# Performance work log

Measured on AMD Instinct MI355X. Metric: run time of the kernel, lower is better.

## Reference

```python
import jax, jax.numpy as jnp
import numpy as np

D_MODEL = 1024
NUM_HEADS = 16
D_K = D_MODEL // NUM_HEADS


def setup_inputs() -> dict:
    key = jax.random.key(0)
    k1, k2, k3, k4 = jax.random.split(key, 4)
    x = jax.random.normal(k1, (2, 2048, D_MODEL), dtype=jnp.float32)
    # qkv_proj: Linear(d_model, 3*d_model, bias=False); stored as [in, out] for x @ W
    W_qkv = jax.random.normal(k2, (D_MODEL, 3 * D_MODEL), dtype=jnp.float32) * (1.0 / np.sqrt(D_MODEL))
    W_out = jax.random.normal(k3, (D_MODEL, D_MODEL), dtype=jnp.float32) * (1.0 / np.sqrt(D_MODEL))
    b_out = jax.random.normal(k4, (D_MODEL,), dtype=jnp.float32) * 0.01
    return {"x": x, "W_qkv": W_qkv, "W_out": W_out, "b_out": b_out}


def reference(x, W_qkv, W_out, b_out):
    B, N, C = x.shape
    scale = 1.0 / np.sqrt(D_K)
    qkv = (x @ W_qkv).reshape(B, N, 3, NUM_HEADS, D_K)
    qkv = jnp.transpose(qkv, (2, 0, 3, 1, 4))  # [3, B, H, N, d_k]
    q, k, v = qkv[0], qkv[1], qkv[2]
    scores = jnp.einsum("bhqd,bhkd->bhqk", q, k) * scale  # [B,H,N,N]
    attn = jax.nn.softmax(scores, axis=-1)
    out = jnp.einsum("bhqk,bhkd->bhqd", attn, v)  # [B,H,N,d_k]
    out = jnp.transpose(out, (0, 2, 1, 3)).reshape(B, N, C)
    return out @ W_out + b_out
```

## Files before the change

kernel.cpp:

```cpp
#include <hip/hip_runtime.h>
#include <cstdint>

typedef __bf16 bf16_t;
typedef __bf16 bf16x4 __attribute__((ext_vector_type(4)));
typedef __bf16 bf16x8 __attribute__((ext_vector_type(8)));
typedef float  f32x4  __attribute__((ext_vector_type(4)));
typedef uint32_t u32x4 __attribute__((ext_vector_type(4)));

#define MFMA16(a,b,c) __builtin_amdgcn_mfma_f32_16x16x32_bf16((a),(b),(c),0,0,0)
#define BAR()    __builtin_amdgcn_s_barrier()
#define VMW(n)   asm volatile("s_waitcnt vmcnt(" #n ")" ::: "memory")

__device__ __forceinline__ void gload_lds16(const bf16_t* g, bf16_t* l) {
  __builtin_amdgcn_global_load_lds(
      (const __attribute__((address_space(1))) unsigned int*)g,
      (__attribute__((address_space(3))) unsigned int*)l,
      16, 0, 0);
}

__device__ __forceinline__ uint32_t cvt_pk_bf16(float lo, float hi) {
  uint32_t r;
  asm("v_cvt_pk_bf16_f32 %0, %1, %2" : "=v"(r) : "v"(lo), "v"(hi));
  return r;
}

__global__ void k_prep(const float* __restrict__ x, bf16_t* __restrict__ xb,
                       const float* __restrict__ Wq, bf16_t* __restrict__ WqT,
                       const float* __restrict__ Wo, bf16_t* __restrict__ WoT) {
  __shared__ float tile[32][33];
  int bid = blockIdx.x;
  if (bid < 2048) {
    int i = bid * blockDim.x + threadIdx.x;
    const float4* p = reinterpret_cast<const float4*>(x) + (size_t)i * 2;
    float4 a = p[0], b = p[1];
    bf16x8 v;
    v[0]=(bf16_t)a.x; v[1]=(bf16_t)a.y; v[2]=(bf16_t)a.z; v[3]=(bf16_t)a.w;
    v[4]=(bf16_t)b.x; v[5]=(bf16_t)b.y; v[6]=(bf16_t)b.z; v[7]=(bf16_t)b.w;
    *reinterpret_cast<bf16x8*>(xb + (size_t)i * 8) = v;
    return;
  }
  int t = bid - 2048;
  int bx = t & 127, k0 = (t >> 7) * 32;
  const float* W; bf16_t* WT; int N, n0;
  if (bx < 96) { W = Wq; WT = WqT; N = 3072; n0 = bx * 32; }
  else         { W = Wo; WT = WoT; N = 1024; n0 = (bx - 96) * 32; }
  int c = threadIdx.x & 31, r8 = threadIdx.x >> 5;
#pragma unroll
  for (int rr = 0; rr < 4; rr++) {
    int r = r8 + rr * 8;
    tile[r][c] = W[(size_t)(k0 + r) * N + n0 + c];
  }
  __syncthreads();
#pragma unroll
  for (int rr = 0; rr < 4; rr++) {
    int r = r8 + rr * 8;
    WT[(size_t)(n0 + r) * 1024 + k0 + c] = (bf16_t)tile[c][r];
  }
}

template<int EPI, int MT, int NT>
__global__ __launch_bounds__(256, 2) void k_gemm(
    const bf16_t* __restrict__ A, const bf16_t* __restrict__ BT, int Klen,
    bf16_t* __restrict__ Qo, bf16_t* __restrict__ Ko, bf16_t* __restrict__ Vt,
    const float* __restrict__ bias, float* __restrict__ Out, int Nout) {
  constexpr int WM = MT / 2;
  constexpr int MF = WM / 16;
  constexpr int WN = NT / 2;
  constexpr int NF = WN / 16;
  __shared__ bf16_t As[2][MT * 32];
  __shared__ bf16_t Bs[2][NT * 32];
  int tid = threadIdx.x, lane = tid & 63, wid = tid >> 6;
  int row0 = blockIdx.x * MT, col0 = blockIdx.y * NT;
  int wr = wid >> 1, wc = wid & 1;
  int g = lane >> 4, li = lane & 15;

  f32x4 acc[MF][NF] = {};

  auto stage = [&](int buf, int kt) {
    int k0 = kt * 32;
#pragma unroll
    for (int j = 0; j < MT / 64; j++) {
      int q = tid + 256 * j;
      int r = q >> 2, part = q & 3;
      gload_lds16(A + (size_t)(row0 + r) * Klen + k0 + part * 8,
                  &As[buf][q * 8]);
    }
#pragma unroll
    for (int j = 0; j < NT / 64; j++) {
      int q = tid + 256 * j;
      int r = q >> 2, part = q & 3;
      gload_lds16(BT + (size_t)(col0 + r) * Klen + k0 + part * 8,
                  &Bs[buf][q * 8]);
    }
  };

  int nk = Klen >> 5;
  stage(0, 0);
  for (int kt = 0; kt < nk; kt++) {
    __syncthreads();
    if (kt + 1 < nk) stage((kt + 1) & 1, kt + 1);
    int buf = kt & 1;
    int kl = g * 8;
    bf16x8 a[MF], b[NF];
#pragma unroll
    for (int m = 0; m < MF; m++)
      a[m] = *reinterpret_cast<const bf16x8*>(&As[buf][(wr * WM + m * 16 + li) * 32 + kl]);
#pragma unroll
    for (int n = 0; n < NF; n++)
      b[n] = *reinterpret_cast<const bf16x8*>(&Bs[buf][(wc * WN + n * 16 + li) * 32 + kl]);
#pragma unroll
    for (int m = 0; m < MF; m++)
#pragma unroll
      for (int n = 0; n < NF; n++)
        acc[m][n] = MFMA16(a[m], b[n], acc[m][n]);
  }

#pragma unroll
  for (int m = 0; m < MF; m++) {
    int rg = row0 + wr * WM + m * 16 + g * 4;
    int b2 = rg >> 11, nn0 = rg & 2047;
#pragma unroll
    for (int n = 0; n < NF; n++) {
      int cg = col0 + wc * WN + n * 16 + li;
      if constexpr (EPI == 0) {
        int t = cg >> 10, h = (cg >> 6) & 15, dk = cg & 63;
        int head = (b2 << 4) + h;
        if (t == 2) {
          bf16x4 pv;
#pragma unroll
          for (int ii = 0; ii < 4; ii++) pv[ii] = (bf16_t)acc[m][n][ii];
          *reinterpret_cast<bf16x4*>(
              &Vt[(size_t)head * 131072 + (size_t)dk * 2048 + nn0]) = pv;
        } else {
#pragma unroll
          for (int ii = 0; ii < 4; ii++) {
            float v = acc[m][n][ii];
            size_t idx = ((size_t)head * 2048 + nn0 + ii) * 64 + dk;
            if (t == 0) Qo[idx] = (bf16_t)(v * 0.18033688011112042f);
            else        Ko[idx] = (bf16_t)v;
          }
        }
      } else {
#pragma unroll
        for (int ii = 0; ii < 4; ii++)
          Out[(size_t)(rg + ii) * Nout + cg] = acc[m][n][ii] + bias[cg];
      }
    }
  }
}

__global__ __launch_bounds__(256, 2) void k_flash(
    const bf16_t* __restrict__ Q, const bf16_t* __restrict__ K,
    const bf16_t* __restrict__ VT, bf16_t* __restrict__ O) {
  __shared__ bf16_t Ks[3][64 * 64];
  __shared__ bf16_t Vs[3][64 * 64];

  int bi = (blockIdx.x & 7) * 64 + (blockIdx.x >> 3);
  int head = bi >> 4, qt = bi & 15;
  int tid = threadIdx.x, lane = tid & 63, wid = tid >> 6;
  int qg = wid >> 1, kg = wid & 1;
  int g = lane >> 4, li = lane & 15;

  const bf16_t* Qh = Q + (size_t)head * 131072 + (size_t)qt * 128 * 64;
  const bf16_t* Kh = K + (size_t)head * 131072;
  const bf16_t* Vh = VT + (size_t)head * 131072;

  bf16x8 qf[4][2];
#pragma unroll
  for (int nq = 0; nq < 4; nq++) {
    const bf16_t* qrow = Qh + (size_t)(qg * 64 + nq * 16 + li) * 64;
    qf[nq][0] = *reinterpret_cast<const bf16x8*>(qrow + g * 8);
    qf[nq][1] = *reinterpret_cast<const bf16x8*>(qrow + 32 + g * 8);
  }

  u32x4 onesw;
  onesw[0] = 0x3F803F80u; onesw[1] = 0x3F803F80u;
  onesw[2] = 0x3F803F80u; onesw[3] = 0x3F803F80u;
  bf16x8 ones = __builtin_bit_cast(bf16x8, onesw);

  f32x4 zero4 = {};
  f32x4 o[4][4] = {};
  f32x4 osum[4] = {};

  auto stage = [&](int buf, int t) {
    int kv0 = t * 64;
#pragma unroll
    for (int j = 0; j < 2; j++) {
      int q = tid + 256 * j;
      int key = q >> 3, part = q & 7;
      int sw = (key & 7) ^ (((key >> 3) & 3) << 1);
      gload_lds16(Kh + (size_t)(kv0 + key) * 64 + ((part ^ sw) * 8),
                  &Ks[buf][(tid + j * 256) * 8]);
    }
#pragma unroll
    for (int j = 0; j < 2; j++) {
      int q = tid + 256 * j;
      int dv = q >> 3, part = q & 7;
      gload_lds16(Vh + (size_t)dv * 2048 + kv0 + ((part ^ (dv & 7)) * 8),
                  &Vs[buf][(tid + j * 256) * 8]);
    }
  };

  stage(0, 0);
  stage(1, 1);
  for (int t = 0; t < 32; t++) {
    if (t < 31) { VMW(4); } else { VMW(0); }
    BAR();
    __builtin_amdgcn_sched_barrier(0);
    if (t + 2 < 32) stage((t + 2) % 3, t + 2);
    int buf = t % 3;
    char* KsB = (char*)&Ks[buf][0];
    char* VsB = (char*)&Vs[buf][0];

    bf16x8 ka[2][2];
#pragma unroll
    for (int kd = 0; kd < 2; kd++)
#pragma unroll
      for (int c = 0; c < 2; c++) {
        int key = kg * 32 + ((li >> 2) << 3) + c * 4 + (li & 3);
        int sw = (key & 7) ^ (((key >> 3) & 3) << 1);
        ka[kd][c] = *reinterpret_cast<const bf16x8*>(
            KsB + key * 128 + (((kd * 4 + g) ^ sw) << 4));
      }

    f32x4 s[2][4];
    __builtin_amdgcn_s_setprio(1);
#pragma unroll
    for (int c = 0; c < 2; c++)
#pragma unroll
      for (int nq = 0; nq < 4; nq++)
        s[c][nq] = MFMA16(ka[0][c], qf[nq][0], zero4);
#pragma unroll
    for (int c = 0; c < 2; c++)
#pragma unroll
      for (int nq = 0; nq < 4; nq++)
        s[c][nq] = MFMA16(ka[1][c], qf[nq][1], s[c][nq]);
    __builtin_amdgcn_s_setprio(0);

    bf16x8 pa[4];
#pragma unroll
    for (int c = 0; c < 2; c++)
#pragma unroll
      for (int nq = 0; nq < 4; nq++)
#pragma unroll
        for (int i = 0; i < 4; i++)
          s[c][nq][i] = __builtin_amdgcn_exp2f(s[c][nq][i]);
#pragma unroll
    for (int nq = 0; nq < 4; nq++) {
      u32x4 w;
      w[0] = cvt_pk_bf16(s[0][nq][0], s[0][nq][1]);
      w[1] = cvt_pk_bf16(s[0][nq][2], s[0][nq][3]);
      w[2] = cvt_pk_bf16(s[1][nq][0], s[1][nq][1]);
      w[3] = cvt_pk_bf16(s[1][nq][2], s[1][nq][3]);
      pa[nq] = __builtin_bit_cast(bf16x8, w);
    }

    __builtin_amdgcn_s_setprio(1);
#pragma unroll
    for (int nq = 0; nq < 4; nq++)
      osum[nq] = MFMA16(pa[nq], ones, osum[nq]);
#pragma unroll
    for (int ndv = 0; ndv < 4; ndv++) {
      int dv = ndv * 16 + li;
      bf16x8 b = *reinterpret_cast<const bf16x8*>(
          VsB + dv * 128 + ((kg * 64 + g * 16) ^ ((dv & 7) << 4)));
#pragma unroll
      for (int nq = 0; nq < 4; nq++)
        o[nq][ndv] = MFMA16(pa[nq], b, o[nq][ndv]);
    }
    __builtin_amdgcn_s_setprio(0);
  }

  __syncthreads();
  float* dump = (float*)&Ks[0][0] + qg * 5120;
  if (kg == 1) {
#pragma unroll
    for (int nq = 0; nq < 4; nq++)
#pragma unroll
      for (int ndv = 0; ndv < 4; ndv++)
#pragma unroll
        for (int i = 0; i < 4; i++)
          dump[(((nq * 4 + ndv) * 4) + i) * 64 + lane] = o[nq][ndv][i];
#pragma unroll
    for (int nq = 0; nq < 4; nq++)
#pragma unroll
      for (int i = 0; i < 4; i++)
        dump[4096 + (nq * 4 + i) * 64 + lane] = osum[nq][i];
  }
  __syncthreads();
  if (kg == 0) {
    int b2 = head >> 4, h = head & 15;
#pragma unroll
    for (int nq = 0; nq < 4; nq++) {
#pragma unroll
      for (int i = 0; i < 4; i++) {
        float ltot = osum[nq][i] + dump[4096 + (nq * 4 + i) * 64 + lane];
        float inv = 1.f / ltot;
        int n = qt * 128 + qg * 64 + nq * 16 + g * 4 + i;
        size_t base = ((size_t)b2 * 2048 + n) * 1024 + h * 64;
#pragma unroll
        for (int ndv = 0; ndv < 4; ndv++) {
          float tot = o[nq][ndv][i] + dump[(((nq * 4 + ndv) * 4) + i) * 64 + lane];
          O[base + ndv * 16 + li] = (bf16_t)(tot * inv);
        }
      }
    }
  }
}

extern "C" void kernel_launch(void* const* d_in, const int* in_sizes, int n_in,
                              void* d_out, int out_size, void* d_ws, size_t ws_size,
                              hipStream_t stream) {
  const float* x    = (const float*)d_in[0];
  const float* Wqkv = (const float*)d_in[1];
  const float* Wout = (const float*)d_in[2];
  const float* bout = (const float*)d_in[3];
  float* out = (float*)d_out;

  char* ws = (char*)d_ws;
  bf16_t* xb    = (bf16_t*)(ws);
  bf16_t* wqkvT = (bf16_t*)(ws + ((size_t)8  << 20));
  bf16_t* woutT = (bf16_t*)(ws + ((size_t)14 << 20));
  bf16_t* qw    = (bf16_t*)(ws + ((size_t)16 << 20));
  bf16_t* kw    = (bf16_t*)(ws + ((size_t)24 << 20));
  bf16_t* vtw   = (bf16_t*)(ws + ((size_t)40 << 20));
  bf16_t* ow    = (bf16_t*)(ws + ((size_t)48 << 20));

  k_prep<<<2048 + 4096, 256, 0, stream>>>(x, xb, Wqkv, wqkvT, Wout, woutT);
  k_gemm<0, 128, 192><<<dim3(32, 16), 256, 0, stream>>>(
      xb, wqkvT, 1024, qw, kw, vtw, nullptr, nullptr, 0);
  k_flash<<<512, 256, 0, stream>>>(qw, kw, vtw, ow);
  k_gemm<1, 64, 128><<<dim3(64, 8), 256, 0, stream>>>(
      ow, woutT, 1024, nullptr, nullptr, nullptr, bout, out, 1024);
}
```

Baseline: 105.6 us.

## Software-pipeline QK of next tile with PV of current tile in flash kernel

Restructures the flash attention loop so the QK^T MFMAs for tile t+1 are issued together with the PV MFMAs for tile t, and the exp/pack of the next tile follows. This is meant to hide exp latency behind matrix work. The LDS ring grows from 3 to 4 buffers and the prefetch distance from 2 to 3, with a prologue and epilogue added. The cost is more LDS per block, which may limit occupancy at 2 blocks per CU, and more live registers.

```diff
diff --git a/kernel.cpp b/kernel.cpp
--- a/kernel.cpp
+++ b/kernel.cpp
@@ -152,8 +152,8 @@
 __global__ __launch_bounds__(256, 2) void k_flash(
     const bf16_t* __restrict__ Q, const bf16_t* __restrict__ K,
     const bf16_t* __restrict__ VT, bf16_t* __restrict__ O) {
-  __shared__ bf16_t Ks[3][64 * 64];
-  __shared__ bf16_t Vs[3][64 * 64];
+  __shared__ bf16_t Ks[4][64 * 64];
+  __shared__ bf16_t Vs[4][64 * 64];
 
   int bi = (blockIdx.x & 7) * 64 + (blockIdx.x >> 3);
   int head = bi >> 4, qt = bi & 15;
@@ -181,6 +181,7 @@
   f32x4 zero4 = {};
   f32x4 o[4][4] = {};
   f32x4 osum[4] = {};
+  bf16x8 pa[4];
 
   auto stage = [&](int buf, int t) {
     int kv0 = t * 64;
@@ -201,18 +202,7 @@
     }
   };
 
-  stage(0, 0);
-  stage(1, 1);
-  for (int t = 0; t < 32; t++) {
-    if (t < 31) { VMW(4); } else { VMW(0); }
-    BAR();
-    __builtin_amdgcn_sched_barrier(0);
-    if (t + 2 < 32) stage((t + 2) % 3, t + 2);
-    int buf = t % 3;
-    char* KsB = (char*)&Ks[buf][0];
-    char* VsB = (char*)&Vs[buf][0];
-
-    bf16x8 ka[2][2];
+  auto read_ka = [&](char* KsB, bf16x8 ka[2][2]) {
 #pragma unroll
     for (int kd = 0; kd < 2; kd++)
 #pragma unroll
@@ -222,9 +212,8 @@
         ka[kd][c] = *reinterpret_cast<const bf16x8*>(
             KsB + key * 128 + (((kd * 4 + g) ^ sw) << 4));
       }
-
-    f32x4 s[2][4];
-    __builtin_amdgcn_s_setprio(1);
+  };
+  auto qk = [&](bf16x8 ka[2][2], f32x4 s[2][4]) {
 #pragma unroll
     for (int c = 0; c < 2; c++)
 #pragma unroll
@@ -235,9 +224,8 @@
 #pragma unroll
       for (int nq = 0; nq < 4; nq++)
         s[c][nq] = MFMA16(ka[1][c], qf[nq][1], s[c][nq]);
-    __builtin_amdgcn_s_setprio(0);
-
-    bf16x8 pa[4];
+  };
+  auto exp_pack = [&](f32x4 s[2][4]) {
 #pragma unroll
     for (int c = 0; c < 2; c++)
 #pragma unroll
@@ -254,22 +242,58 @@
       w[3] = cvt_pk_bf16(s[1][nq][2], s[1][nq][3]);
       pa[nq] = __builtin_bit_cast(bf16x8, w);
     }
-
-    __builtin_amdgcn_s_setprio(1);
+  };
+  auto pv = [&](char* VsB) {
+    bf16x8 vb[4];
+#pragma unroll
+    for (int ndv = 0; ndv < 4; ndv++) {
+      int dv = ndv * 16 + li;
+      vb[ndv] = *reinterpret_cast<const bf16x8*>(
+          VsB + dv * 128 + ((kg * 64 + g * 16) ^ ((dv & 7) << 4)));
+    }
 #pragma unroll
     for (int nq = 0; nq < 4; nq++)
       osum[nq] = MFMA16(pa[nq], ones, osum[nq]);
 #pragma unroll
-    for (int ndv = 0; ndv < 4; ndv++) {
-      int dv = ndv * 16 + li;
-      bf16x8 b = *reinterpret_cast<const bf16x8*>(
-          VsB + dv * 128 + ((kg * 64 + g * 16) ^ ((dv & 7) << 4)));
+    for (int ndv = 0; ndv < 4; ndv++)
 #pragma unroll
       for (int nq = 0; nq < 4; nq++)
-        o[nq][ndv] = MFMA16(pa[nq], b, o[nq][ndv]);
-    }
+        o[nq][ndv] = MFMA16(pa[nq], vb[ndv], o[nq][ndv]);
+  };
+
+  stage(0, 0); stage(1, 1); stage(2, 2);
+  VMW(8); BAR();
+  __builtin_amdgcn_sched_barrier(0);
+  {
+    bf16x8 ka[2][2];
+    f32x4 s[2][4];
+    read_ka((char*)&Ks[0][0], ka);
+    __builtin_amdgcn_s_setprio(1);
+    qk(ka, s);
     __builtin_amdgcn_s_setprio(0);
-  }
+    exp_pack(s);
+  }
+
+  for (int t = 0; t < 31; t++) {
+    if (t < 30) { VMW(4); } else { VMW(0); }
+    BAR();
+    __builtin_amdgcn_sched_barrier(0);
+    if (t + 3 < 32) stage((t + 3) & 3, t + 3);
+
+    char* KsB = (char*)&Ks[(t + 1) & 3][0];
+    char* VsB = (char*)&Vs[t & 3][0];
+
+    bf16x8 ka[2][2];
+    f32x4 s[2][4];
+    read_ka(KsB, ka);
+    __builtin_amdgcn_s_setprio(1);
+    qk(ka, s);
+    pv(VsB);
+    __builtin_amdgcn_s_setprio(0);
+    exp_pack(s);
+  }
+
+  { pv((char*)&Vs[31 & 3][0]); }
 
   __syncthreads();
   float* dump = (float*)&Ks[0][0] + qg * 5120;
```

Result: no change. 107.1 us (+1.4%).

## Load K/V fragments directly from global into registers, dropping LDS staging

Applied to the files above, without the earlier changes.

The flash attention kernel no longer stages K and V tiles through triple-buffered shared memory with barriers. Each wave loads its K and V MFMA operand fragments straight from global memory into registers, double-buffering K in registers and loading V one step ahead. This removes the LDS writes and reads and the per-tile block barriers, at the cost of redundant global/L2 traffic, since both query-group waves load the same K/V, and of exposed global-load latency with a shallow prefetch. LDS is now used only for the final cross-wave reduction.

```diff
diff --git a/kernel.cpp b/kernel.cpp
--- a/kernel.cpp
+++ b/kernel.cpp
@@ -8,8 +8,6 @@
 typedef uint32_t u32x4 __attribute__((ext_vector_type(4)));
 
 #define MFMA16(a,b,c) __builtin_amdgcn_mfma_f32_16x16x32_bf16((a),(b),(c),0,0,0)
-#define BAR()    __builtin_amdgcn_s_barrier()
-#define VMW(n)   asm volatile("s_waitcnt vmcnt(" #n ")" ::: "memory")
 
 __device__ __forceinline__ void gload_lds16(const bf16_t* g, bf16_t* l) {
   __builtin_amdgcn_global_load_lds(
@@ -152,8 +150,7 @@
 __global__ __launch_bounds__(256, 2) void k_flash(
     const bf16_t* __restrict__ Q, const bf16_t* __restrict__ K,
     const bf16_t* __restrict__ VT, bf16_t* __restrict__ O) {
-  __shared__ bf16_t Ks[3][64 * 64];
-  __shared__ bf16_t Vs[3][64 * 64];
+  __shared__ float dumpS[2][5120];
 
   int bi = (blockIdx.x & 7) * 64 + (blockIdx.x >> 3);
   int head = bi >> 4, qt = bi & 15;
@@ -181,48 +178,34 @@
   f32x4 zero4 = {};
   f32x4 o[4][4] = {};
   f32x4 osum[4] = {};
-
-  auto stage = [&](int buf, int t) {
-    int kv0 = t * 64;
-#pragma unroll
-    for (int j = 0; j < 2; j++) {
-      int q = tid + 256 * j;
-      int key = q >> 3, part = q & 7;
-      int sw = (key & 7) ^ (((key >> 3) & 3) << 1);
-      gload_lds16(Kh + (size_t)(kv0 + key) * 64 + ((part ^ sw) * 8),
-                  &Ks[buf][(tid + j * 256) * 8]);
-    }
-#pragma unroll
-    for (int j = 0; j < 2; j++) {
-      int q = tid + 256 * j;
-      int dv = q >> 3, part = q & 7;
-      gload_lds16(Vh + (size_t)dv * 2048 + kv0 + ((part ^ (dv & 7)) * 8),
-                  &Vs[buf][(tid + j * 256) * 8]);
-    }
-  };
-
-  stage(0, 0);
-  stage(1, 1);
-  for (int t = 0; t < 32; t++) {
-    if (t < 31) { VMW(4); } else { VMW(0); }
-    BAR();
-    __builtin_amdgcn_sched_barrier(0);
-    if (t + 2 < 32) stage((t + 2) % 3, t + 2);
-    int buf = t % 3;
-    char* KsB = (char*)&Ks[buf][0];
-    char* VsB = (char*)&Vs[buf][0];
-
-    bf16x8 ka[2][2];
+  bf16x8 pa[4];
+
+  const bf16_t* kp[2][2];
+#pragma unroll
+  for (int kd = 0; kd < 2; kd++)
+#pragma unroll
+    for (int c = 0; c < 2; c++) {
+      int key = kg * 32 + ((li >> 2) << 3) + c * 4 + (li & 3);
+      kp[kd][c] = Kh + (size_t)key * 64 + kd * 32 + g * 8;
+    }
+  const bf16_t* vp[4];
+#pragma unroll
+  for (int ndv = 0; ndv < 4; ndv++)
+    vp[ndv] = Vh + (size_t)(ndv * 16 + li) * 2048 + kg * 32 + g * 8;
+
+  auto loadK = [&](bf16x8 ka[2][2], int t) {
 #pragma unroll
     for (int kd = 0; kd < 2; kd++)
 #pragma unroll
-      for (int c = 0; c < 2; c++) {
-        int key = kg * 32 + ((li >> 2) << 3) + c * 4 + (li & 3);
-        int sw = (key & 7) ^ (((key >> 3) & 3) << 1);
-        ka[kd][c] = *reinterpret_cast<const bf16x8*>(
-            KsB + key * 128 + (((kd * 4 + g) ^ sw) << 4));
-      }
-
+      for (int c = 0; c < 2; c++)
+        ka[kd][c] = *reinterpret_cast<const bf16x8*>(kp[kd][c] + (size_t)t * 4096);
+  };
+  auto loadV = [&](bf16x8 vb[4], int t) {
+#pragma unroll
+    for (int ndv = 0; ndv < 4; ndv++)
+      vb[ndv] = *reinterpret_cast<const bf16x8*>(vp[ndv] + t * 64);
+  };
+  auto qkpack = [&](bf16x8 ka[2][2]) {
     f32x4 s[2][4];
     __builtin_amdgcn_s_setprio(1);
 #pragma unroll
@@ -236,8 +219,6 @@
       for (int nq = 0; nq < 4; nq++)
         s[c][nq] = MFMA16(ka[1][c], qf[nq][1], s[c][nq]);
     __builtin_amdgcn_s_setprio(0);
-
-    bf16x8 pa[4];
 #pragma unroll
     for (int c = 0; c < 2; c++)
 #pragma unroll
@@ -254,25 +235,36 @@
       w[3] = cvt_pk_bf16(s[1][nq][2], s[1][nq][3]);
       pa[nq] = __builtin_bit_cast(bf16x8, w);
     }
-
+  };
+  auto pv = [&](bf16x8 vb[4]) {
     __builtin_amdgcn_s_setprio(1);
 #pragma unroll
     for (int nq = 0; nq < 4; nq++)
       osum[nq] = MFMA16(pa[nq], ones, osum[nq]);
 #pragma unroll
-    for (int ndv = 0; ndv < 4; ndv++) {
-      int dv = ndv * 16 + li;
-      bf16x8 b = *reinterpret_cast<const bf16x8*>(
-          VsB + dv * 128 + ((kg * 64 + g * 16) ^ ((dv & 7) << 4)));
+    for (int ndv = 0; ndv < 4; ndv++)
 #pragma unroll
       for (int nq = 0; nq < 4; nq++)
-        o[nq][ndv] = MFMA16(pa[nq], b, o[nq][ndv]);
-    }
+        o[nq][ndv] = MFMA16(pa[nq], vb[ndv], o[nq][ndv]);
     __builtin_amdgcn_s_setprio(0);
+  };
+
+  bf16x8 kaA[2][2], kaB[2][2], vb[4];
+  loadK(kaA, 0);
+  loadK(kaB, 1);
+  for (int t = 0; t < 32; t += 2) {
+    loadV(vb, t);
+    qkpack(kaA);
+    if (t + 2 < 32) loadK(kaA, t + 2);
+    pv(vb);
+    loadV(vb, t + 1);
+    qkpack(kaB);
+    if (t + 3 < 32) loadK(kaB, t + 3);
+    pv(vb);
   }
 
   __syncthreads();
-  float* dump = (float*)&Ks[0][0] + qg * 5120;
+  float* dump = &dumpS[qg][0];
   if (kg == 1) {
 #pragma unroll
     for (int nq = 0; nq < 4; nq++)
```

Result: slower. 130.3 us (+23.4%).
